# Kernel tuning notes

Measured on AMD Instinct MI355X. Metric: run time of the kernel, lower is better.

Reference implementation:

```python
import jax, jax.numpy as jnp
import numpy as np

DIM = 512
HEADS = 8
DIM_HEAD = 64
INNER = HEADS * DIM_HEAD  # 512
EPS = 1e-6


def setup_inputs() -> dict:
    key = jax.random.key(0)
    ks = jax.random.split(key, 6)
    B, N = 8, 2048
    x = jax.random.normal(ks[0], (B, N, DIM), dtype=jnp.float32)
    # nn.Linear stores weight as [out, in]; we keep that layout and transpose in matmul.
    w_qkv = jax.random.normal(ks[1], (3 * INNER, DIM), dtype=jnp.float32) * (1.0 / np.sqrt(DIM))
    w_proj = jax.random.normal(ks[2], (DIM, INNER), dtype=jnp.float32) * (1.0 / np.sqrt(INNER))
    b_proj = jax.random.normal(ks[3], (DIM,), dtype=jnp.float32) * 0.01
    ln_gamma = jnp.ones((DIM,), dtype=jnp.float32)
    ln_beta = jnp.zeros((DIM,), dtype=jnp.float32)
    return {"x": x, "w_qkv": w_qkv, "w_proj": w_proj, "b_proj": b_proj,
            "ln_gamma": ln_gamma, "ln_beta": ln_beta}


def reference(x, w_qkv, w_proj, b_proj, ln_gamma, ln_beta):
    B, N, D = x.shape
    H, Dh = HEADS, DIM_HEAD
    # LayerNorm (eps=1e-6)
    mu = jnp.mean(x, axis=-1, keepdims=True)
    var = jnp.mean(jnp.square(x - mu), axis=-1, keepdims=True)
    xn = (x - mu) * jax.lax.rsqrt(var + EPS) * ln_gamma + ln_beta
    # QKV projection (no bias)
    qkv = xn @ w_qkv.T  # [B, N, 3*INNER]
    q, k, v = jnp.split(qkv, 3, axis=-1)
    # [B, N, H, Dh] -> [B, H, N, Dh]
    q = q.reshape(B, N, H, Dh).transpose(0, 2, 1, 3)
    k = k.reshape(B, N, H, Dh).transpose(0, 2, 1, 3)
    v = v.reshape(B, N, H, Dh).transpose(0, 2, 1, 3)
    scale = Dh ** (-0.5)
    attn = jnp.einsum('bhnd,bhmd->bhnm', q, k) * scale  # [B, H, N, N]
    attn = jax.nn.softmax(attn, axis=-1)
    out = jnp.einsum('bhnm,bhmd->bhnd', attn, v)  # [B, H, N, Dh]
    out = out.transpose(0, 2, 1, 3).reshape(B, N, H * Dh)
    out = out @ w_proj.T + b_proj
    return out
```

## Files before the change

### kernel.cpp

```cpp
#include <hip/hip_runtime.h>

typedef unsigned short u16;
typedef __bf16 bf16x8 __attribute__((ext_vector_type(8)));
typedef float f32x4 __attribute__((ext_vector_type(4)));
typedef float f32x16 __attribute__((ext_vector_type(16)));

#define DIMD 512
#define SEQN 2048
#define NB   8
#define NH   8
#define DH   64
#define BHN  (NB*NH)
#define MROWS (NB*SEQN)
#define QSCALE 0.18033688f

__device__ __forceinline__ u16 f2bf(float f) {
  union { float f; unsigned u; } x; x.f = f;
  unsigned r = x.u + 0x7fffu + ((x.u >> 16) & 1u);
  return (u16)(r >> 16);
}

__device__ __forceinline__ void gll16(const u16* g, u16* lbase) {
#if __has_builtin(__builtin_amdgcn_global_load_lds)
  __builtin_amdgcn_global_load_lds(
      (const __attribute__((address_space(1))) unsigned int*)g,
      (__attribute__((address_space(3))) unsigned int*)lbase, 16, 0, 0);
#else
  *(uint4*)((u16*)lbase + (threadIdx.x & 63) * 8) = *(const uint4*)g;
#endif
}

__device__ __forceinline__ bf16x8 mkfrag(float e0, float e1, float e2, float e3,
                                          float e4, float e5, float e6, float e7) {
  unsigned a0, a1, a2, a3;
  asm("v_cvt_pk_bf16_f32 %0, %1, %2" : "=v"(a0) : "v"(e0), "v"(e1));
  asm("v_cvt_pk_bf16_f32 %0, %1, %2" : "=v"(a1) : "v"(e2), "v"(e3));
  asm("v_cvt_pk_bf16_f32 %0, %1, %2" : "=v"(a2) : "v"(e4), "v"(e5));
  asm("v_cvt_pk_bf16_f32 %0, %1, %2" : "=v"(a3) : "v"(e6), "v"(e7));
  asm volatile("v_permlane32_swap_b32 %0, %1" : "+v"(a0), "+v"(a2));
  asm volatile("v_permlane32_swap_b32 %0, %1" : "+v"(a1), "+v"(a3));
  union { unsigned u[4]; bf16x8 v; } r;
  r.u[0] = a0; r.u[1] = a1; r.u[2] = a2; r.u[3] = a3;
  return r.v;
}

__global__ __launch_bounds__(256) void wcvt2(
    const float* __restrict__ wa, const float* __restrict__ wb,
    u16* __restrict__ oa, u16* __restrict__ ob, int na, int nb) {
  int i = (blockIdx.x * 256 + threadIdx.x) * 8;
  const float* src; u16* dst; int idx;
  if (i < na) { src = wa; dst = oa; idx = i; }
  else { idx = i - na; if (idx >= nb) return; src = wb; dst = ob; }
  float4 f0 = *(const float4*)(src + idx);
  float4 f1 = *(const float4*)(src + idx + 4);
  union { uint4 v; u16 s[8]; } u;
  u.s[0] = f2bf(f0.x); u.s[1] = f2bf(f0.y); u.s[2] = f2bf(f0.z); u.s[3] = f2bf(f0.w);
  u.s[4] = f2bf(f1.x); u.s[5] = f2bf(f1.y); u.s[6] = f2bf(f1.z); u.s[7] = f2bf(f1.w);
  *(uint4*)(dst + idx) = u.v;
}

__global__ __launch_bounds__(256) void ln_kernel(
    const float* __restrict__ x, const float* __restrict__ gamma,
    const float* __restrict__ beta, u16* __restrict__ xn) {
  int row = blockIdx.x * 4 + (threadIdx.x >> 6);
  int lane = threadIdx.x & 63;
  const float* xr = x + (size_t)row * DIMD;
  float f[8], g[8], b[8];
  *(float4*)&f[0] = *(const float4*)(xr + lane * 8);
  *(float4*)&f[4] = *(const float4*)(xr + lane * 8 + 4);
  *(float4*)&g[0] = *(const float4*)(gamma + lane * 8);
  *(float4*)&g[4] = *(const float4*)(gamma + lane * 8 + 4);
  *(float4*)&b[0] = *(const float4*)(beta + lane * 8);
  *(float4*)&b[4] = *(const float4*)(beta + lane * 8 + 4);
  float sum = 0.f, sq = 0.f;
#pragma unroll
  for (int i = 0; i < 8; ++i) { sum += f[i]; sq += f[i] * f[i]; }
#pragma unroll
  for (int off = 1; off < 64; off <<= 1) {
    sum += __shfl_xor(sum, off, 64);
    sq  += __shfl_xor(sq, off, 64);
  }
  float mean = sum * (1.0f / DIMD);
  float var = sq * (1.0f / DIMD) - mean * mean;
  float rstd = rsqrtf(var + 1e-6f);
  union { uint4 v; u16 s[8]; } uo;
#pragma unroll
  for (int i = 0; i < 8; ++i)
    uo.s[i] = f2bf((f[i] - mean) * rstd * g[i] + b[i]);
  *(uint4*)(xn + (size_t)row * DIMD + lane * 8) = uo.v;
}

__global__ __launch_bounds__(256) void qkv_gemm(
    const u16* __restrict__ A, const u16* __restrict__ Bm,
    u16* __restrict__ qo, u16* __restrict__ ko, u16* __restrict__ vto) {
  __shared__ __align__(16) u16 la[128 * 64];
  __shared__ __align__(16) u16 lb[128 * 64];
  const int K = DIMD;
  int tid = threadIdx.x;
  int bm = blockIdx.x, bn = blockIdx.y;
  int wid = tid >> 6, lane = tid & 63, lm = lane & 15, quad = lane >> 4;
  int wm = wid >> 1, wn = wid & 1;
  int lsw = lm & 7;
  int part = bn >> 2;
  f32x4 acc[4][4] = {};
  const u16* Ab = A + (size_t)(bm * 128) * K;
  const u16* Bb = Bm + (size_t)(bn * 128) * K;
  int cb_row = lane >> 3, cb_sub = lane & 7;
  int xsrc = (cb_sub ^ cb_row) * 8;
  for (int k0 = 0; k0 < K; k0 += 64) {
    __syncthreads();
#pragma unroll
    for (int r = 0; r < 4; ++r) {
      int seg = wid * 4 + r;
      int row = seg * 8 + cb_row;
      size_t goff = (size_t)row * K + k0 + xsrc;
      gll16(Ab + goff, &la[seg * 512]);
      gll16(Bb + goff, &lb[seg * 512]);
    }
    __syncthreads();
#pragma unroll
    for (int h = 0; h < 2; ++h) {
      bf16x8 af[4], bfr[4];
#pragma unroll
      for (int i = 0; i < 4; ++i)
        af[i] = *(const bf16x8*)&la[(wm * 64 + i * 16 + lm) * 64 + (((h * 4 + quad) ^ lsw) * 8)];
#pragma unroll
      for (int j = 0; j < 4; ++j)
        bfr[j] = *(const bf16x8*)&lb[(wn * 64 + j * 16 + lm) * 64 + (((h * 4 + quad) ^ lsw) * 8)];
      if (part == 2) {
#pragma unroll
        for (int i = 0; i < 4; ++i)
#pragma unroll
          for (int j = 0; j < 4; ++j)
            acc[i][j] = __builtin_amdgcn_mfma_f32_16x16x32_bf16(af[i], bfr[j], acc[i][j], 0, 0, 0);
      } else {
#pragma unroll
        for (int i = 0; i < 4; ++i)
#pragma unroll
          for (int j = 0; j < 4; ++j)
            acc[i][j] = __builtin_amdgcn_mfma_f32_16x16x32_bf16(bfr[j], af[i], acc[i][j], 0, 0, 0);
      }
    }
  }
  if (part == 2) {
#pragma unroll
    for (int i = 0; i < 4; ++i)
#pragma unroll
      for (int j = 0; j < 4; ++j) {
        int col = bn * 128 + wn * 64 + j * 16 + lm;
        int rem = col & 511, h = rem >> 6, d = rem & 63;
        int rg = bm * 128 + wm * 64 + i * 16 + quad * 4;
        int b = rg >> 11, nn = rg & 2047;
        union { unsigned long long ll; u16 s4[4]; } pk;
#pragma unroll
        for (int r = 0; r < 4; ++r) pk.s4[r] = f2bf(acc[i][j][r]);
        *(unsigned long long*)&vto[((size_t)(b * NH + h) * DH + d) * SEQN + nn] = pk.ll;
      }
  } else {
    u16* dst = part ? ko : qo;
    float sc = part ? 1.0f : QSCALE;
#pragma unroll
    for (int i = 0; i < 4; ++i)
#pragma unroll
      for (int j = 0; j < 4; ++j) {
        int rg = bm * 128 + wm * 64 + i * 16 + lm;
        int b = rg >> 11, nn = rg & 2047;
        int col = bn * 128 + wn * 64 + j * 16 + quad * 4;
        int rem = col & 511, hh = rem >> 6, d = rem & 63;
        union { unsigned long long ll; __bf16 h4[4]; } pk;
#pragma unroll
        for (int r = 0; r < 4; ++r) pk.h4[r] = (__bf16)(acc[i][j][r] * sc);
        *(unsigned long long*)&dst[((size_t)(b * NH + hh) * SEQN + nn) * DH + d] = pk.ll;
      }
  }
}

__global__ __launch_bounds__(512, 4) void attn_kernel(
    const u16* __restrict__ q, const u16* __restrict__ k,
    const u16* __restrict__ vt, u16* __restrict__ att) {
  __shared__ __align__(16) u16 kt[2][64 * 64];
  __shared__ __align__(16) u16 vtt[2][64 * 64];
  int bh = blockIdx.x;
  int wid = threadIdx.x >> 6, lane = threadIdx.x & 63;
  int l31 = lane & 31, hi = lane >> 5;
  int qrow0 = blockIdx.y * 256 + wid * 32;
  const u16* qb = q + (size_t)bh * SEQN * DH;
  const u16* kb = k + (size_t)bh * SEQN * DH;
  const u16* vb = vt + (size_t)bh * DH * SEQN;

  int cb_row = lane >> 3, cb_sub = lane & 7;
  int xstage = (cb_sub ^ cb_row) * 8;

  bf16x8 ones;
#pragma unroll
  for (int i = 0; i < 8; ++i) ones[i] = (__bf16)1.0f;

  bf16x8 qf[4];
#pragma unroll
  for (int c = 0; c < 4; ++c)
    qf[c] = *(const bf16x8*)(qb + (size_t)(qrow0 + l31) * DH + c * 16 + hi * 8);

  f32x16 Ot0 = {}, Ot1 = {};
  f32x16 lacc = {};

  auto stage = [&](int bsel, int j0) {
    if (wid < 4) {
#pragma unroll
      for (int i = 0; i < 2; ++i) {
        int seg = wid * 2 + i;
        int row = seg * 8 + cb_row;
        gll16(kb + (size_t)(j0 + row) * DH + xstage, &kt[bsel][seg * 512]);
      }
    } else {
#pragma unroll
      for (int i = 0; i < 2; ++i) {
        int seg = (wid - 4) * 2 + i;
        int row = seg * 8 + cb_row;
        gll16(vb + (size_t)row * SEQN + j0 + xstage, &vtt[bsel][seg * 512]);
      }
    }
  };

  stage(0, 0);
  for (int t = 0; t < SEQN / 64; ++t) {
    int bsel = t & 1;
    __syncthreads();
    if (t + 1 < SEQN / 64) stage(bsel ^ 1, (t + 1) * 64);

    bf16x8 pb[4];
#pragma unroll
    for (int tb = 0; tb < 2; ++tb) {
      int row = tb * 32 + l31;
      int rsw = row & 7;
      f32x16 z = {};
      __builtin_amdgcn_s_setprio(1);
#pragma unroll
      for (int c = 0; c < 4; ++c) {
        bf16x8 kf = *(const bf16x8*)&kt[bsel][row * 64 + (((2 * c + hi) ^ rsw) * 8)];
        z = __builtin_amdgcn_mfma_f32_32x32x16_bf16(kf, qf[c], z, 0, 0, 0);
      }
      __builtin_amdgcn_s_setprio(0);
      float e[16];
#pragma unroll
      for (int r = 0; r < 16; ++r) e[r] = __builtin_amdgcn_exp2f(z[r]);
      pb[tb * 2 + 0] = mkfrag(e[0], e[1], e[2], e[3], e[4], e[5], e[6], e[7]);
      pb[tb * 2 + 1] = mkfrag(e[8], e[9], e[10], e[11], e[12], e[13], e[14], e[15]);
    }
    __builtin_amdgcn_s_setprio(1);
    lacc = __builtin_amdgcn_mfma_f32_32x32x16_bf16(ones, pb[0], lacc, 0, 0, 0);
    lacc = __builtin_amdgcn_mfma_f32_32x32x16_bf16(ones, pb[1], lacc, 0, 0, 0);
    lacc = __builtin_amdgcn_mfma_f32_32x32x16_bf16(ones, pb[2], lacc, 0, 0, 0);
    lacc = __builtin_amdgcn_mfma_f32_32x32x16_bf16(ones, pb[3], lacc, 0, 0, 0);
    __builtin_amdgcn_s_setprio(0);
    int rsw0 = l31 & 7;
#pragma unroll
    for (int c = 0; c < 4; ++c) {
      bf16x8 va0 = *(const bf16x8*)&vtt[bsel][l31 * 64 + (((2 * c + hi) ^ rsw0) * 8)];
      bf16x8 va1 = *(const bf16x8*)&vtt[bsel][(32 + l31) * 64 + (((2 * c + hi) ^ rsw0) * 8)];
      __builtin_amdgcn_s_setprio(1);
      Ot0 = __builtin_amdgcn_mfma_f32_32x32x16_bf16(va0, pb[c], Ot0, 0, 0, 0);
      Ot1 = __builtin_amdgcn_mfma_f32_32x32x16_bf16(va1, pb[c], Ot1, 0, 0, 0);
      __builtin_amdgcn_s_setprio(0);
    }
  }
  int b = bh >> 3, h = bh & 7;
  float inv = __builtin_amdgcn_rcpf(lacc[0]);
  size_t rowoff = ((size_t)(b * SEQN + qrow0 + l31)) * DIMD + h * DH;
#pragma unroll
  for (int rb = 0; rb < 4; ++rb) {
    union { unsigned long long ll; __bf16 h4[4]; } o0, o1;
#pragma unroll
    for (int rr = 0; rr < 4; ++rr) {
      o0.h4[rr] = (__bf16)(Ot0[rb * 4 + rr] * inv);
      o1.h4[rr] = (__bf16)(Ot1[rb * 4 + rr] * inv);
    }
    *(unsigned long long*)&att[rowoff + rb * 8 + hi * 4] = o0.ll;
    *(unsigned long long*)&att[rowoff + 32 + rb * 8 + hi * 4] = o1.ll;
  }
}

__global__ __launch_bounds__(256) void proj_gemm(
    const u16* __restrict__ A, const u16* __restrict__ Bm,
    const float* __restrict__ bias, float* __restrict__ C) {
  __shared__ __align__(16) u16 la[128 * 64];
  __shared__ __align__(16) u16 lb[128 * 64];
  const int K = DIMD, N = DIMD;
  int tid = threadIdx.x;
  int bm = blockIdx.x, bn = blockIdx.y;
  int wid = tid >> 6, lane = tid & 63, lm = lane & 15, quad = lane >> 4;
  int wm = wid >> 1, wn = wid & 1;
  int lsw = lm & 7;
  f32x4 acc[4][4] = {};
  const u16* Ab = A + (size_t)(bm * 128) * K;
  const u16* Bb = Bm + (size_t)(bn * 128) * K;
  int cb_row = lane >> 3, cb_sub = lane & 7;
  int xsrc = (cb_sub ^ cb_row) * 8;
  for (int k0 = 0; k0 < K; k0 += 64) {
    __syncthreads();
#pragma unroll
    for (int r = 0; r < 4; ++r) {
      int seg = wid * 4 + r;
      int row = seg * 8 + cb_row;
      size_t goff = (size_t)row * K + k0 + xsrc;
      gll16(Ab + goff, &la[seg * 512]);
      gll16(Bb + goff, &lb[seg * 512]);
    }
    __syncthreads();
#pragma unroll
    for (int h = 0; h < 2; ++h) {
      bf16x8 af[4], bfr[4];
#pragma unroll
      for (int i = 0; i < 4; ++i)
        af[i] = *(const bf16x8*)&la[(wm * 64 + i * 16 + lm) * 64 + (((h * 4 + quad) ^ lsw) * 8)];
#pragma unroll
      for (int j = 0; j < 4; ++j)
        bfr[j] = *(const bf16x8*)&lb[(wn * 64 + j * 16 + lm) * 64 + (((h * 4 + quad) ^ lsw) * 8)];
#pragma unroll
      for (int i = 0; i < 4; ++i)
#pragma unroll
        for (int j = 0; j < 4; ++j)
          acc[i][j] = __builtin_amdgcn_mfma_f32_16x16x32_bf16(bfr[j], af[i], acc[i][j], 0, 0, 0);
    }
  }
#pragma unroll
  for (int i = 0; i < 4; ++i)
#pragma unroll
    for (int j = 0; j < 4; ++j) {
      int rg = bm * 128 + wm * 64 + i * 16 + lm;
      int col = bn * 128 + wn * 64 + j * 16 + quad * 4;
      float4 bv = *(const float4*)(bias + col);
      float4 o;
      o.x = acc[i][j][0] + bv.x; o.y = acc[i][j][1] + bv.y;
      o.z = acc[i][j][2] + bv.z; o.w = acc[i][j][3] + bv.w;
      *(float4*)&C[(size_t)rg * N + col] = o;
    }
}

extern "C" void kernel_launch(void* const* d_in, const int* in_sizes, int n_in,
                              void* d_out, int out_size, void* d_ws, size_t ws_size,
                              hipStream_t stream) {
  const float* x      = (const float*)d_in[0];
  const float* w_qkv  = (const float*)d_in[1];
  const float* w_proj = (const float*)d_in[2];
  const float* b_proj = (const float*)d_in[3];
  const float* gamma  = (const float*)d_in[4];
  const float* beta   = (const float*)d_in[5];
  float* out = (float*)d_out;

  const size_t SZ = (size_t)MROWS * DIMD;
  u16* xn  = (u16*)d_ws;
  u16* q   = xn + SZ;
  u16* kk  = q + SZ;
  u16* vt  = kk + SZ;
  u16* wqb = vt + SZ;
  u16* wpb = wqb + (size_t)3 * DIMD * DIMD;
  u16* att = xn;

  const int NQKV = 3 * DIMD * DIMD;
  const int NPRJ = DIMD * DIMD;
  wcvt2<<<dim3((NQKV + NPRJ) / 2048), dim3(256), 0, stream>>>(
      w_qkv, w_proj, wqb, wpb, NQKV, NPRJ);
  ln_kernel<<<dim3(MROWS / 4), dim3(256), 0, stream>>>(x, gamma, beta, xn);
  qkv_gemm<<<dim3(MROWS / 128, (3 * DIMD) / 128), dim3(256), 0, stream>>>(
      xn, wqb, q, kk, vt);
  attn_kernel<<<dim3(BHN, SEQN / 256), dim3(512), 0, stream>>>(q, kk, vt, att);
  proj_gemm<<<dim3(MROWS / 128, DIMD / 128), dim3(256), 0, stream>>>(
      att, wpb, b_proj, out);
}
```

Before: 227.3 us.

## Give each attention wave two query tiles and sum softmax denominators with VALU adds

```diff
diff --git a/kernel.cpp b/kernel.cpp
--- a/kernel.cpp
+++ b/kernel.cpp
@@ -175,7 +175,7 @@
   }
 }
 
-__global__ __launch_bounds__(512, 4) void attn_kernel(
+__global__ __launch_bounds__(256, 2) void attn_kernel(
     const u16* __restrict__ q, const u16* __restrict__ k,
     const u16* __restrict__ vt, u16* __restrict__ att) {
   __shared__ __align__(16) u16 kt[2][64 * 64];
@@ -183,7 +183,7 @@
   int bh = blockIdx.x;
   int wid = threadIdx.x >> 6, lane = threadIdx.x & 63;
   int l31 = lane & 31, hi = lane >> 5;
-  int qrow0 = blockIdx.y * 256 + wid * 32;
+  int qrow0 = blockIdx.y * 256 + wid * 64;
   const u16* qb = q + (size_t)bh * SEQN * DH;
   const u16* kb = k + (size_t)bh * SEQN * DH;
   const u16* vb = vt + (size_t)bh * DH * SEQN;
@@ -191,30 +191,28 @@
   int cb_row = lane >> 3, cb_sub = lane & 7;
   int xstage = (cb_sub ^ cb_row) * 8;
 
-  bf16x8 ones;
-#pragma unroll
-  for (int i = 0; i < 8; ++i) ones[i] = (__bf16)1.0f;
-
-  bf16x8 qf[4];
-#pragma unroll
-  for (int c = 0; c < 4; ++c)
-    qf[c] = *(const bf16x8*)(qb + (size_t)(qrow0 + l31) * DH + c * 16 + hi * 8);
-
-  f32x16 Ot0 = {}, Ot1 = {};
-  f32x16 lacc = {};
+  bf16x8 qfA[4], qfB[4];
+#pragma unroll
+  for (int c = 0; c < 4; ++c) {
+    qfA[c] = *(const bf16x8*)(qb + (size_t)(qrow0 + l31) * DH + c * 16 + hi * 8);
+    qfB[c] = *(const bf16x8*)(qb + (size_t)(qrow0 + 32 + l31) * DH + c * 16 + hi * 8);
+  }
+
+  f32x16 OtA0 = {}, OtA1 = {}, OtB0 = {}, OtB1 = {};
+  float lA = 0.f, lB = 0.f;
 
   auto stage = [&](int bsel, int j0) {
-    if (wid < 4) {
-#pragma unroll
-      for (int i = 0; i < 2; ++i) {
-        int seg = wid * 2 + i;
+    if (wid < 2) {
+#pragma unroll
+      for (int i = 0; i < 4; ++i) {
+        int seg = wid * 4 + i;
         int row = seg * 8 + cb_row;
         gll16(kb + (size_t)(j0 + row) * DH + xstage, &kt[bsel][seg * 512]);
       }
     } else {
 #pragma unroll
-      for (int i = 0; i < 2; ++i) {
-        int seg = (wid - 4) * 2 + i;
+      for (int i = 0; i < 4; ++i) {
+        int seg = (wid - 2) * 4 + i;
         int row = seg * 8 + cb_row;
         gll16(vb + (size_t)row * SEQN + j0 + xstage, &vtt[bsel][seg * 512]);
       }
@@ -227,55 +225,64 @@
     __syncthreads();
     if (t + 1 < SEQN / 64) stage(bsel ^ 1, (t + 1) * 64);
 
-    bf16x8 pb[4];
+    bf16x8 pbA[4], pbB[4];
+    int rsw = l31 & 7;
 #pragma unroll
     for (int tb = 0; tb < 2; ++tb) {
       int row = tb * 32 + l31;
-      int rsw = row & 7;
-      f32x16 z = {};
+      f32x16 zA = {}, zB = {};
       __builtin_amdgcn_s_setprio(1);
 #pragma unroll
       for (int c = 0; c < 4; ++c) {
         bf16x8 kf = *(const bf16x8*)&kt[bsel][row * 64 + (((2 * c + hi) ^ rsw) * 8)];
-        z = __builtin_amdgcn_mfma_f32_32x32x16_bf16(kf, qf[c], z, 0, 0, 0);
+        zA = __builtin_amdgcn_mfma_f32_32x32x16_bf16(kf, qfA[c], zA, 0, 0, 0);
+        zB = __builtin_amdgcn_mfma_f32_32x32x16_bf16(kf, qfB[c], zB, 0, 0, 0);
       }
       __builtin_amdgcn_s_setprio(0);
-      float e[16];
-#pragma unroll
-      for (int r = 0; r < 16; ++r) e[r] = __builtin_amdgcn_exp2f(z[r]);
-      pb[tb * 2 + 0] = mkfrag(e[0], e[1], e[2], e[3], e[4], e[5], e[6], e[7]);
-      pb[tb * 2 + 1] = mkfrag(e[8], e[9], e[10], e[11], e[12], e[13], e[14], e[15]);
-    }
-    __builtin_amdgcn_s_setprio(1);
-    lacc = __builtin_amdgcn_mfma_f32_32x32x16_bf16(ones, pb[0], lacc, 0, 0, 0);
-    lacc = __builtin_amdgcn_mfma_f32_32x32x16_bf16(ones, pb[1], lacc, 0, 0, 0);
-    lacc = __builtin_amdgcn_mfma_f32_32x32x16_bf16(ones, pb[2], lacc, 0, 0, 0);
-    lacc = __builtin_amdgcn_mfma_f32_32x32x16_bf16(ones, pb[3], lacc, 0, 0, 0);
-    __builtin_amdgcn_s_setprio(0);
-    int rsw0 = l31 & 7;
+      float eA[16], eB[16];
+#pragma unroll
+      for (int r = 0; r < 16; ++r) {
+        eA[r] = __builtin_amdgcn_exp2f(zA[r]); lA += eA[r];
+        eB[r] = __builtin_amdgcn_exp2f(zB[r]); lB += eB[r];
+      }
+      pbA[tb * 2 + 0] = mkfrag(eA[0], eA[1], eA[2], eA[3], eA[4], eA[5], eA[6], eA[7]);
+      pbA[tb * 2 + 1] = mkfrag(eA[8], eA[9], eA[10], eA[11], eA[12], eA[13], eA[14], eA[15]);
+      pbB[tb * 2 + 0] = mkfrag(eB[0], eB[1], eB[2], eB[3], eB[4], eB[5], eB[6], eB[7]);
+      pbB[tb * 2 + 1] = mkfrag(eB[8], eB[9], eB[10], eB[11], eB[12], eB[13], eB[14], eB[15]);
+    }
 #pragma unroll
     for (int c = 0; c < 4; ++c) {
-      bf16x8 va0 = *(const bf16x8*)&vtt[bsel][l31 * 64 + (((2 * c + hi) ^ rsw0) * 8)];
-      bf16x8 va1 = *(const bf16x8*)&vtt[bsel][(32 + l31) * 64 + (((2 * c + hi) ^ rsw0) * 8)];
+      bf16x8 va0 = *(const bf16x8*)&vtt[bsel][l31 * 64 + (((2 * c + hi) ^ rsw) * 8)];
+      bf16x8 va1 = *(const bf16x8*)&vtt[bsel][(32 + l31) * 64 + (((2 * c + hi) ^ rsw) * 8)];
       __builtin_amdgcn_s_setprio(1);
-      Ot0 = __builtin_amdgcn_mfma_f32_32x32x16_bf16(va0, pb[c], Ot0, 0, 0, 0);
-      Ot1 = __builtin_amdgcn_mfma_f32_32x32x16_bf16(va1, pb[c], Ot1, 0, 0, 0);
+      OtA0 = __builtin_amdgcn_mfma_f32_32x32x16_bf16(va0, pbA[c], OtA0, 0, 0, 0);
+      OtA1 = __builtin_amdgcn_mfma_f32_32x32x16_bf16(va1, pbA[c], OtA1, 0, 0, 0);
+      OtB0 = __builtin_amdgcn_mfma_f32_32x32x16_bf16(va0, pbB[c], OtB0, 0, 0, 0);
+      OtB1 = __builtin_amdgcn_mfma_f32_32x32x16_bf16(va1, pbB[c], OtB1, 0, 0, 0);
       __builtin_amdgcn_s_setprio(0);
     }
   }
   int b = bh >> 3, h = bh & 7;
-  float inv = __builtin_amdgcn_rcpf(lacc[0]);
-  size_t rowoff = ((size_t)(b * SEQN + qrow0 + l31)) * DIMD + h * DH;
+  float lAf = lA + __shfl_xor(lA, 32, 64);
+  float lBf = lB + __shfl_xor(lB, 32, 64);
+  float invA = __builtin_amdgcn_rcpf(lAf);
+  float invB = __builtin_amdgcn_rcpf(lBf);
+  size_t rowA = ((size_t)(b * SEQN + qrow0 + l31)) * DIMD + h * DH;
+  size_t rowB = ((size_t)(b * SEQN + qrow0 + 32 + l31)) * DIMD + h * DH;
 #pragma unroll
   for (int rb = 0; rb < 4; ++rb) {
-    union { unsigned long long ll; __bf16 h4[4]; } o0, o1;
+    union { unsigned long long ll; __bf16 h4[4]; } a0, a1, b0, b1;
 #pragma unroll
     for (int rr = 0; rr < 4; ++rr) {
-      o0.h4[rr] = (__bf16)(Ot0[rb * 4 + rr] * inv);
-      o1.h4[rr] = (__bf16)(Ot1[rb * 4 + rr] * inv);
-    }
-    *(unsigned long long*)&att[rowoff + rb * 8 + hi * 4] = o0.ll;
-    *(unsigned long long*)&att[rowoff + 32 + rb * 8 + hi * 4] = o1.ll;
+      a0.h4[rr] = (__bf16)(OtA0[rb * 4 + rr] * invA);
+      a1.h4[rr] = (__bf16)(OtA1[rb * 4 + rr] * invA);
+      b0.h4[rr] = (__bf16)(OtB0[rb * 4 + rr] * invB);
+      b1.h4[rr] = (__bf16)(OtB1[rb * 4 + rr] * invB);
+    }
+    *(unsigned long long*)&att[rowA + rb * 8 + hi * 4] = a0.ll;
+    *(unsigned long long*)&att[rowA + 32 + rb * 8 + hi * 4] = a1.ll;
+    *(unsigned long long*)&att[rowB + rb * 8 + hi * 4] = b0.ll;
+    *(unsigned long long*)&att[rowB + 32 + rb * 8 + hi * 4] = b1.ll;
   }
 }
 
@@ -363,7 +370,7 @@
   ln_kernel<<<dim3(MROWS / 4), dim3(256), 0, stream>>>(x, gamma, beta, xn);
   qkv_gemm<<<dim3(MROWS / 128, (3 * DIMD) / 128), dim3(256), 0, stream>>>(
       xn, wqb, q, kk, vt);
-  attn_kernel<<<dim3(BHN, SEQN / 256), dim3(512), 0, stream>>>(q, kk, vt, att);
+  attn_kernel<<<dim3(BHN, SEQN / 256), dim3(256), 0, stream>>>(q, kk, vt, att);
   proj_gemm<<<dim3(MROWS / 128, DIMD / 128), dim3(256), 0, stream>>>(
       att, wpb, b_proj, out);
 }
```

Result: faster. 220.4 us (-3.0%).
